# Performance work log

Measured on AMD Instinct MI355X. Metric: run time of the kernel, lower is better.

## Reference

```python
import jax, jax.numpy as jnp
import numpy as np

N = 50000      # nodes
E = 400000     # edges (before self-loops)
IN = 128
HID = 64
HEADS = 8
OUT = 3
NEG_SLOPE = 0.2
EPS = 1e-6


def setup_inputs() -> dict:
    key = jax.random.key(0)
    ks = jax.random.split(key, 32)
    def nrm(k, shape, s=0.05):
        return jax.random.normal(k, shape, dtype=jnp.float32) * s
    inp = {}
    inp['x'] = nrm(ks[0], (N, IN), 1.0)
    inp['edge_index'] = jax.random.randint(ks[1], (2, E), 0, N)
    inp['res_W'] = nrm(ks[2], (OUT, IN))
    inp['res_b'] = jnp.zeros((OUT,), jnp.float32)
    # (in, out, heads, concat) per GAT layer
    dims = [(IN, HID, HEADS, True), (HID * HEADS, HID, HEADS, True),
            (HID * HEADS, HID, HEADS, True), (HID * HEADS, OUT, 1, False)]
    j = 3
    for i, (ci, co, h, cc) in enumerate(dims):
        inp['ln_g%d' % i] = jnp.ones((ci,), jnp.float32)
        inp['ln_b%d' % i] = jnp.zeros((ci,), jnp.float32)
        inp['W%d' % i] = nrm(ks[j], (h * co, ci)); j += 1
        inp['asr%d' % i] = nrm(ks[j], (h, co)); j += 1
        inp['adt%d' % i] = nrm(ks[j], (h, co)); j += 1
        inp['b%d' % i] = jnp.zeros((h * co if cc else co,), jnp.float32)
    return inp


def layer_norm(x, g, b):
    mu = x.mean(-1, keepdims=True)
    var = ((x - mu) ** 2).mean(-1, keepdims=True)
    return (x - mu) / jnp.sqrt(var + EPS) * g + b


def gat_conv(x, src, dst, W, a_src, a_dst, bias, heads, co, concat):
    n = x.shape[0]
    h = (x @ W.T).reshape(n, heads, co)                    # [N,H,C]
    al_src = jnp.sum(h * a_src, axis=-1)                   # [N,H]
    al_dst = jnp.sum(h * a_dst, axis=-1)                   # [N,H]
    e = jax.nn.leaky_relu(al_src[src] + al_dst[dst], NEG_SLOPE)  # [E',H]
    # segment softmax over incoming edges of each destination node
    m = jax.ops.segment_max(e, dst, num_segments=n)
    e = jnp.exp(e - m[dst])
    s = jax.ops.segment_sum(e, dst, num_segments=n)
    alpha = e / s[dst]                                     # [E',H]
    msg = h[src] * alpha[..., None]                        # [E',H,C]
    out = jax.ops.segment_sum(msg, dst, num_segments=n)    # [N,H,C]
    out = out.reshape(n, heads * co) if concat else out.mean(axis=1)
    return out + bias


def reference(x, edge_index, res_W, res_b,
              ln_g0, ln_b0, W0, asr0, adt0, b0,
              ln_g1, ln_b1, W1, asr1, adt1, b1,
              ln_g2, ln_b2, W2, asr2, adt2, b2,
              ln_g3, ln_b3, W3, asr3, adt3, b3):
    n = x.shape[0]
    loops = jnp.arange(n)
    src = jnp.concatenate([edge_index[0], loops])          # add self-loops (PyG default)
    dst = jnp.concatenate([edge_index[1], loops])
    residual = x @ res_W.T + res_b
    layers = [(ln_g0, ln_b0, W0, asr0, adt0, b0, HEADS, HID, True),
              (ln_g1, ln_b1, W1, asr1, adt1, b1, HEADS, HID, True),
              (ln_g2, ln_b2, W2, asr2, adt2, b2, HEADS, HID, True),
              (ln_g3, ln_b3, W3, asr3, adt3, b3, 1, OUT, False)]
    h = x
    num_layers = len(layers)
    for i, (g, bb, W, a_s, a_d, bi, hd, co, cc) in enumerate(layers):
        x_res = h
        h = layer_norm(h, g, bb)
        h = gat_conv(h, src, dst, W, a_s, a_d, bi, hd, co, cc)
        if i < num_layers - 1:
            h = jax.nn.gelu(h, approximate=False)
            if h.shape == x_res.shape:
                h = h + x_res
    return h + residual
```

## Files before the change

kernel.cpp:

```cpp
#include <hip/hip_runtime.h>
#include <math.h>

#define NN 50000
#define MPAD 50048
#define EE 400000
#define NE 450000
#define IN_F 128
#define NEG_SLOPE 0.2f
#define EPSV 1e-6f

typedef unsigned short bf16u;
typedef short bf8_t __attribute__((ext_vector_type(8)));
typedef float f32x4 __attribute__((ext_vector_type(4)));

__device__ __forceinline__ float bf2f(unsigned int u) {
    return __uint_as_float(u << 16);
}
__device__ __forceinline__ float bf2f_hi(unsigned int u) {
    return __uint_as_float(u & 0xFFFF0000u);
}
__device__ __forceinline__ bf16u f2bf(float f) {
    unsigned int u = __float_as_uint(f);
    unsigned int r = (u + 0x7FFFu + ((u >> 16) & 1u)) >> 16;
    return (bf16u)r;
}
__device__ __forceinline__ float gelu_f(float v) {
    return 0.5f * v * (1.0f + erff(v * 0.70710678118654752f));
}

__device__ __forceinline__ void gload_lds16(const void* g, void* l) {
    __builtin_amdgcn_global_load_lds(
        (__attribute__((address_space(1))) void*)(g),
        (__attribute__((address_space(3))) void*)(l), 16, 0, 0);
}

__global__ void k_zero_i32(int* p, int n) {
    int i = blockIdx.x * 256 + threadIdx.x;
    if (i < n) p[i] = 0;
}

__global__ void k_deg(const int* __restrict__ ei, int* __restrict__ deg) {
    int i = blockIdx.x * 256 + threadIdx.x;
    if (i >= NE) return;
    int d = (i < EE) ? ei[EE + i] : (i - EE);
    atomicAdd(&deg[d], 1);
}

__global__ __launch_bounds__(256) void k_scan1(const int* __restrict__ deg,
                                               int* __restrict__ incl,
                                               int* __restrict__ bsums, int n) {
    __shared__ int sm[1024];
    int base = blockIdx.x * 1024;
    for (int i = threadIdx.x; i < 1024; i += 256)
        sm[i] = (base + i < n) ? deg[base + i] : 0;
    __syncthreads();
    for (int off = 1; off < 1024; off <<= 1) {
        int v[4];
#pragma unroll
        for (int j = 0; j < 4; j++) {
            int i = threadIdx.x + 256 * j;
            v[j] = (i >= off) ? sm[i - off] : 0;
        }
        __syncthreads();
#pragma unroll
        for (int j = 0; j < 4; j++) {
            int i = threadIdx.x + 256 * j;
            sm[i] += v[j];
        }
        __syncthreads();
    }
    for (int i = threadIdx.x; i < 1024; i += 256)
        if (base + i < n) incl[base + i] = sm[i];
    if (threadIdx.x == 0) bsums[blockIdx.x] = sm[1023];
}

__global__ void k_scan2(int* bsums, int nb) {
    if (threadIdx.x == 0 && blockIdx.x == 0) {
        int run = 0;
        for (int i = 0; i < nb; i++) { int v = bsums[i]; bsums[i] = run; run += v; }
    }
}

__global__ void k_scan3(const int* __restrict__ deg, int* __restrict__ rowptr,
                        int* __restrict__ cursor, const int* __restrict__ bsums,
                        int n, int ne) {
    int i = blockIdx.x * 256 + threadIdx.x;
    if (i < n) {
        int excl = rowptr[i] + bsums[i >> 10] - deg[i];
        rowptr[i] = excl;
        cursor[i] = excl;
    }
    if (i == n) rowptr[n] = ne;
}

__global__ void k_scatter(const int* __restrict__ ei, int* __restrict__ cursor,
                          int* __restrict__ col) {
    int i = blockIdx.x * 256 + threadIdx.x;
    if (i >= NE) return;
    int s, d;
    if (i < EE) { s = ei[i]; d = ei[EE + i]; }
    else        { s = i - EE; d = i - EE; }
    int p = atomicAdd(&cursor[d], 1);
    col[p] = s;
}

__global__ void k_cast(const float* __restrict__ x, bf16u* __restrict__ h, int total) {
    int i = blockIdx.x * 256 + threadIdx.x;
    if (i < total) h[i] = f2bf(x[i]);
}

__global__ __launch_bounds__(256) void k_castres(const float* __restrict__ x,
                                                 const float* __restrict__ rw,
                                                 const float* __restrict__ rb,
                                                 bf16u* __restrict__ h,
                                                 float* __restrict__ stats,
                                                 float* __restrict__ res, int n) {
    int row = (blockIdx.x * 256 + threadIdx.x) >> 6;
    int lane = threadIdx.x & 63;
    if (row >= n) return;
    float2 v = *(const float2*)(x + (size_t)row * 128 + lane * 2);
    unsigned int pk = (unsigned int)f2bf(v.x) | ((unsigned int)f2bf(v.y) << 16);
    *(unsigned int*)(h + (size_t)row * 128 + lane * 2) = pk;
    float2 w0 = *(const float2*)(rw + 0 * 128 + lane * 2);
    float2 w1 = *(const float2*)(rw + 1 * 128 + lane * 2);
    float2 w2 = *(const float2*)(rw + 2 * 128 + lane * 2);
    float s = v.x + v.y, s2 = v.x * v.x + v.y * v.y;
    float a0 = v.x * w0.x + v.y * w0.y;
    float a1 = v.x * w1.x + v.y * w1.y;
    float a2 = v.x * w2.x + v.y * w2.y;
#pragma unroll
    for (int off = 32; off; off >>= 1) {
        s  += __shfl_xor(s, off);
        s2 += __shfl_xor(s2, off);
        a0 += __shfl_xor(a0, off);
        a1 += __shfl_xor(a1, off);
        a2 += __shfl_xor(a2, off);
    }
    if (lane == 0) {
        float mu = s * (1.0f / 128.0f);
        float var = s2 * (1.0f / 128.0f) - mu * mu;
        stats[row * 2 + 0] = mu;
        stats[row * 2 + 1] = rsqrtf(var + EPSV);
        res[row * 3 + 0] = a0 + rb[0];
        res[row * 3 + 1] = a1 + rb[1];
        res[row * 3 + 2] = a2 + rb[2];
    }
}

#define BM 128
#define BN 128
#define BKK 32
__global__ __launch_bounds__(256) void k_gemm_mfma(const bf16u* __restrict__ H,
                                                   const float* __restrict__ stats,
                                                   const float* __restrict__ g,
                                                   const float* __restrict__ bbias,
                                                   const bf16u* __restrict__ Wb,
                                                   bf16u* __restrict__ C,
                                                   const float* __restrict__ asr,
                                                   const float* __restrict__ adt,
                                                   float* __restrict__ alsrc,
                                                   float* __restrict__ aldst,
                                                   int Mreal, int ci, int K) {
    __shared__ __align__(16) bf16u As[BM * BKK];
    __shared__ __align__(16) bf16u Bs[BN * BKK];
    const int tid = threadIdx.x;
    const int w = tid >> 6, lane = tid & 63;
    const int row0 = blockIdx.x * BM, col0 = blockIdx.y * BN;
    const int wr = (w >> 1) * 64, wc = (w & 1) * 64;

    const int srow = w * 32 + (lane >> 2);
    const int scol = (lane & 3) * 8;
    const bf16u* gA = H + (size_t)(row0 + srow) * ci + scol;
    const bf16u* gB = Wb + (size_t)(col0 + srow) * ci + scol;
    const float mu1 = stats[(row0 + srow) * 2 + 0];
    const float rs1 = stats[(row0 + srow) * 2 + 1];
    const float mu2 = stats[(row0 + srow + 16) * 2 + 0];
    const float rs2 = stats[(row0 + srow + 16) * 2 + 1];
    bf16u* lA1 = &As[(size_t)srow * BKK + scol];
    bf16u* lA2 = &As[(size_t)(srow + 16) * BKK + scol];
    void* lB1 = &Bs[(size_t)(w * 32) * BKK];
    void* lB2 = &Bs[(size_t)(w * 32 + 16) * BKK];

    f32x4 acc[4][4] = {};

    const int fr = lane & 15;
    const int fk = (lane >> 4) * 8;

    for (int k0 = 0; k0 < ci; k0 += BKK) {
        uint4 ra1 = *(const uint4*)(gA + k0);
        uint4 ra2 = *(const uint4*)(gA + (size_t)16 * ci + k0);
        float4 g0 = *(const float4*)(g + k0 + scol);
        float4 g1 = *(const float4*)(g + k0 + scol + 4);
        float4 b0 = *(const float4*)(bbias + k0 + scol);
        float4 b1 = *(const float4*)(bbias + k0 + scol + 4);
        float gg[8] = {g0.x, g0.y, g0.z, g0.w, g1.x, g1.y, g1.z, g1.w};
        float bb[8] = {b0.x, b0.y, b0.z, b0.w, b1.x, b1.y, b1.z, b1.w};
        unsigned int u1[4] = {ra1.x, ra1.y, ra1.z, ra1.w};
        unsigned int u2[4] = {ra2.x, ra2.y, ra2.z, ra2.w};
        uint4 p1, p2;
        {
            unsigned int po[4], qo[4];
#pragma unroll
            for (int j = 0; j < 4; j++) {
                float va = (bf2f(u1[j] & 0xFFFFu) - mu1) * rs1;
                float vb = (bf2f_hi(u1[j])         - mu1) * rs1;
                float oa = fmaf(va, gg[2 * j], bb[2 * j]);
                float ob = fmaf(vb, gg[2 * j + 1], bb[2 * j + 1]);
                po[j] = (unsigned int)f2bf(oa) | ((unsigned int)f2bf(ob) << 16);
                float vc = (bf2f(u2[j] & 0xFFFFu) - mu2) * rs2;
                float vd = (bf2f_hi(u2[j])         - mu2) * rs2;
                float oc = fmaf(vc, gg[2 * j], bb[2 * j]);
                float od = fmaf(vd, gg[2 * j + 1], bb[2 * j + 1]);
                qo[j] = (unsigned int)f2bf(oc) | ((unsigned int)f2bf(od) << 16);
            }
            p1 = make_uint4(po[0], po[1], po[2], po[3]);
            p2 = make_uint4(qo[0], qo[1], qo[2], qo[3]);
        }

        __syncthreads();
        *(uint4*)lA1 = p1;
        *(uint4*)lA2 = p2;
        gload_lds16(gB + k0, lB1);
        gload_lds16(gB + (size_t)16 * ci + k0, lB2);
        __syncthreads();

        bf8_t af[4], bf[4];
#pragma unroll
        for (int m = 0; m < 4; m++)
            af[m] = *(const bf8_t*)&As[(size_t)(wr + m * 16 + fr) * BKK + fk];
#pragma unroll
        for (int n = 0; n < 4; n++)
            bf[n] = *(const bf8_t*)&Bs[(size_t)(wc + n * 16 + fr) * BKK + fk];
#pragma unroll
        for (int m = 0; m < 4; m++)
#pragma unroll
            for (int n = 0; n < 4; n++)
                acc[m][n] = __builtin_amdgcn_mfma_f32_16x16x32_bf16(af[m], bf[n], acc[m][n], 0, 0, 0);
    }

    const int fc = lane & 15;
    const int fq = (lane >> 4) * 4;

#pragma unroll
    for (int m = 0; m < 4; m++) {
#pragma unroll
        for (int r = 0; r < 4; r++) {
            int row = row0 + wr + m * 16 + fq + r;
            if (row >= Mreal) continue;
#pragma unroll
            for (int n = 0; n < 4; n++) {
                int col = col0 + wc + n * 16 + fc;
                C[(size_t)row * K + col] = f2bf(acc[m][n][r]);
            }
        }
    }

    const int head = blockIdx.y * 2 + (wc >> 6);
    float av[4], dv[4];
#pragma unroll
    for (int n = 0; n < 4; n++) {
        av[n] = asr[head * 64 + n * 16 + fc];
        dv[n] = adt[head * 64 + n * 16 + fc];
    }
#pragma unroll
    for (int m = 0; m < 4; m++) {
#pragma unroll
        for (int r = 0; r < 4; r++) {
            float s1 = acc[m][0][r] * av[0] + acc[m][1][r] * av[1]
                     + acc[m][2][r] * av[2] + acc[m][3][r] * av[3];
            float s2 = acc[m][0][r] * dv[0] + acc[m][1][r] * dv[1]
                     + acc[m][2][r] * dv[2] + acc[m][3][r] * dv[3];
#pragma unroll
            for (int o = 1; o < 16; o <<= 1) {
                s1 += __shfl_xor(s1, o);
                s2 += __shfl_xor(s2, o);
            }
            int row = row0 + wr + m * 16 + fq + r;
            if (fc == 0 && row < Mreal) {
                alsrc[row * 8 + head] = s1;
                aldst[row * 8 + head] = s2;
            }
        }
    }
}

__global__ __launch_bounds__(256) void k_lin3(const bf16u* __restrict__ h,
                                              const float* __restrict__ stats,
                                              const float* __restrict__ g,
                                              const float* __restrict__ bb,
                                              const float* __restrict__ W,
                                              const float* __restrict__ a_s,
                                              const float* __restrict__ a_d,
                                              bf16u* __restrict__ hlin3,
                                              float* __restrict__ alsrc,
                                              float* __restrict__ aldst, int n) {
    int row = (blockIdx.x * 256 + threadIdx.x) >> 6;
    int lane = threadIdx.x & 63;
    if (row >= n) return;
    float mu = stats[row * 2 + 0], rs = stats[row * 2 + 1];
    uint4 r = *(const uint4*)(h + (size_t)row * 512 + lane * 8);
    float4 g0 = *(const float4*)(g + lane * 8);
    float4 g1 = *(const float4*)(g + lane * 8 + 4);
    float4 b0 = *(const float4*)(bb + lane * 8);
    float4 b1 = *(const float4*)(bb + lane * 8 + 4);
    float gg[8] = {g0.x, g0.y, g0.z, g0.w, g1.x, g1.y, g1.z, g1.w};
    float bv[8] = {b0.x, b0.y, b0.z, b0.w, b1.x, b1.y, b1.z, b1.w};
    unsigned int u[4] = {r.x, r.y, r.z, r.w};
    float ln[8];
#pragma unroll
    for (int j = 0; j < 4; j++) {
        ln[2 * j]     = fmaf((bf2f(u[j] & 0xFFFFu) - mu) * rs, gg[2 * j], bv[2 * j]);
        ln[2 * j + 1] = fmaf((bf2f_hi(u[j])         - mu) * rs, gg[2 * j + 1], bv[2 * j + 1]);
    }
    float a0 = 0.f, a1 = 0.f, a2 = 0.f;
#pragma unroll
    for (int j = 0; j < 8; j++) {
        int k = lane * 8 + j;
        a0 += ln[j] * W[k];
        a1 += ln[j] * W[512 + k];
        a2 += ln[j] * W[1024 + k];
    }
#pragma unroll
    for (int off = 32; off; off >>= 1) {
        a0 += __shfl_down(a0, off);
        a1 += __shfl_down(a1, off);
        a2 += __shfl_down(a2, off);
    }
    if (lane == 0) {
        *(unsigned int*)(hlin3 + (size_t)row * 4) =
            (unsigned int)f2bf(a0) | ((unsigned int)f2bf(a1) << 16);
        *(unsigned int*)(hlin3 + (size_t)row * 4 + 2) = (unsigned int)f2bf(a2);
        alsrc[row] = a0 * a_s[0] + a1 * a_s[1] + a2 * a_s[2];
        aldst[row] = a0 * a_d[0] + a1 * a_d[1] + a2 * a_d[2];
    }
}

__global__ __launch_bounds__(256) void k_aggN(const bf16u* __restrict__ hlin,
                                              const float* __restrict__ alsrc,
                                              const float* __restrict__ aldst,
                                              const int* __restrict__ rowptr,
                                              const int* __restrict__ col,
                                              const float* __restrict__ bias,
                                              bf16u* __restrict__ hio,
                                              float* __restrict__ stats,
                                              int n, int dores) {
    __shared__ uint2 aldsU[4][8][66];
    int wv = threadIdx.x >> 6;
    int node = (blockIdx.x * 256 + threadIdx.x) >> 6;
    int lane = threadIdx.x & 63;
    if (node >= n) return;
    int beg = rowptr[node], end = rowptr[node + 1];
    int deg = end - beg;

    const float4* dvv = (const float4*)(aldst + node * 8);
    float4 da = dvv[0], db = dvv[1];
    float ad[8] = {da.x, da.y, da.z, da.w, db.x, db.y, db.z, db.w};

    float s = 0.f, s2 = 0.f;

    if (deg <= 64) {
        unsigned int offb = 0;
        float raw[8];
#pragma unroll
        for (int h = 0; h < 8; h++) raw[h] = -INFINITY;
        if (lane < deg) {
            int srcreg = col[beg + lane];
            offb = (unsigned int)srcreg << 10;
            const float4* sv = (const float4*)(alsrc + srcreg * 8);
            float4 sa = sv[0], sb = sv[1];
            float sl[8] = {sa.x, sa.y, sa.z, sa.w, sb.x, sb.y, sb.z, sb.w};
#pragma unroll
            for (int h = 0; h < 8; h++) {
                float v = sl[h] + ad[h];
                raw[h] = (v >= 0.f) ? v : NEG_SLOPE * v;
            }
        }
        float m[8];
#pragma unroll
        for (int h = 0; h < 8; h++) m[h] = raw[h];
#pragma unroll
        for (int off = 32; off; off >>= 1)
#pragma unroll
            for (int h = 0; h < 8; h++) m[h] = fmaxf(m[h], __shfl_xor(m[h], off));
        float ex[8], sm[8];
#pragma unroll
        for (int h = 0; h < 8; h++) {
            ex[h] = (lane < deg) ? __expf(raw[h] - m[h]) : 0.f;
            sm[h] = ex[h];
        }
#pragma unroll
        for (int off = 32; off; off >>= 1)
#pragma unroll
            for (int h = 0; h < 8; h++) sm[h] += __shfl_xor(sm[h], off);
#pragma unroll
        for (int h = 0; h < 8; h++) {
            uint2 t;
            t.x = __float_as_uint(ex[h] * (1.0f / sm[h]));
            t.y = offb;
            aldsU[wv][h][lane] = t;
        }
        asm volatile("s_waitcnt lgkmcnt(0)" ::: "memory");

        int hl = lane >> 3;
        const uint2* myal = &aldsU[wv][hl][0];
        const char* base2 = (const char*)hlin + (lane << 4);
        float acc[8] = {};
        int e = 0;
        for (; e + 2 <= deg; e += 2) {
            uint2 t0 = myal[e];
            uint2 t1 = myal[e + 1];
            uint4 u0 = *(const uint4*)(base2 + t0.y);
            uint4 u1 = *(const uint4*)(base2 + t1.y);
            float a0 = __uint_as_float(t0.x), a1 = __uint_as_float(t1.x);
            acc[0] = fmaf(a0, bf2f(u0.x & 0xFFFFu), acc[0]);
            acc[1] = fmaf(a0, bf2f_hi(u0.x),        acc[1]);
            acc[2] = fmaf(a0, bf2f(u0.y & 0xFFFFu), acc[2]);
            acc[3] = fmaf(a0, bf2f_hi(u0.y),        acc[3]);
            acc[4] = fmaf(a0, bf2f(u0.z & 0xFFFFu), acc[4]);
            acc[5] = fmaf(a0, bf2f_hi(u0.z),        acc[5]);
            acc[6] = fmaf(a0, bf2f(u0.w & 0xFFFFu), acc[6]);
            acc[7] = fmaf(a0, bf2f_hi(u0.w),        acc[7]);
            acc[0] = fmaf(a1, bf2f(u1.x & 0xFFFFu), acc[0]);
            acc[1] = fmaf(a1, bf2f_hi(u1.x),        acc[1]);
            acc[2] = fmaf(a1, bf2f(u1.y & 0xFFFFu), acc[2]);
            acc[3] = fmaf(a1, bf2f_hi(u1.y),        acc[3]);
            acc[4] = fmaf(a1, bf2f(u1.z & 0xFFFFu), acc[4]);
            acc[5] = fmaf(a1, bf2f_hi(u1.z),        acc[5]);
            acc[6] = fmaf(a1, bf2f(u1.w & 0xFFFFu), acc[6]);
            acc[7] = fmaf(a1, bf2f_hi(u1.w),        acc[7]);
        }
        if (e < deg) {
            uint2 t0 = myal[e];
            uint4 u0 = *(const uint4*)(base2 + t0.y);
            float a0 = __uint_as_float(t0.x);
            acc[0] = fmaf(a0, bf2f(u0.x & 0xFFFFu), acc[0]);
            acc[1] = fmaf(a0, bf2f_hi(u0.x),        acc[1]);
            acc[2] = fmaf(a0, bf2f(u0.y & 0xFFFFu), acc[2]);
            acc[3] = fmaf(a0, bf2f_hi(u0.y),        acc[3]);
            acc[4] = fmaf(a0, bf2f(u0.z & 0xFFFFu), acc[4]);
            acc[5] = fmaf(a0, bf2f_hi(u0.z),        acc[5]);
            acc[6] = fmaf(a0, bf2f(u0.w & 0xFFFFu), acc[6]);
            acc[7] = fmaf(a0, bf2f_hi(u0.w),        acc[7]);
        }

        size_t idx = (size_t)node * 512 + lane * 8;
        float4 b0 = *(const float4*)(bias + lane * 8);
        float4 b1 = *(const float4*)(bias + lane * 8 + 4);
        float bb[8] = {b0.x, b0.y, b0.z, b0.w, b1.x, b1.y, b1.z, b1.w};
        float fin[8];
#pragma unroll
        for (int j = 0; j < 8; j++) fin[j] = gelu_f(acc[j] + bb[j]);
        if (dores) {
            uint4 up = *(const uint4*)(hio + idx);
            fin[0] += bf2f(up.x & 0xFFFFu); fin[1] += bf2f_hi(up.x);
            fin[2] += bf2f(up.y & 0xFFFFu); fin[3] += bf2f_hi(up.y);
            fin[4] += bf2f(up.z & 0xFFFFu); fin[5] += bf2f_hi(up.z);
            fin[6] += bf2f(up.w & 0xFFFFu); fin[7] += bf2f_hi(up.w);
        }
        uint4 pk;
        pk.x = (unsigned int)f2bf(fin[0]) | ((unsigned int)f2bf(fin[1]) << 16);
        pk.y = (unsigned int)f2bf(fin[2]) | ((unsigned int)f2bf(fin[3]) << 16);
        pk.z = (unsigned int)f2bf(fin[4]) | ((unsigned int)f2bf(fin[5]) << 16);
        pk.w = (unsigned int)f2bf(fin[6]) | ((unsigned int)f2bf(fin[7]) << 16);
        *(uint4*)(hio + idx) = pk;
#pragma unroll
        for (int j = 0; j < 8; j++) { s += fin[j]; s2 += fin[j] * fin[j]; }
    } else {
        for (int h = 0; h < 8; h++) {
            float adh = ad[h];
            float m = -INFINITY;
            for (int e = beg + lane; e < end; e += 64) {
                float v = alsrc[col[e] * 8 + h] + adh;
                v = (v >= 0.f) ? v : NEG_SLOPE * v;
                m = fmaxf(m, v);
            }
#pragma unroll
            for (int off = 32; off; off >>= 1) m = fmaxf(m, __shfl_xor(m, off));
            float sum = 0.f;
            for (int e = beg + lane; e < end; e += 64) {
                float v = alsrc[col[e] * 8 + h] + adh;
                v = (v >= 0.f) ? v : NEG_SLOPE * v;
                sum += __expf(v - m);
            }
#pragma unroll
            for (int off = 32; off; off >>= 1) sum += __shfl_xor(sum, off);
            float inv = 1.0f / sum;
            float acc = 0.f;
            for (int e = beg; e < end; e++) {
                int src = col[e];
                float v = alsrc[src * 8 + h] + adh;
                v = (v >= 0.f) ? v : NEG_SLOPE * v;
                float alpha = __expf(v - m) * inv;
                acc = fmaf(alpha, bf2f(hlin[((size_t)src << 9) + h * 64 + lane]), acc);
            }
            float fin = gelu_f(acc + bias[h * 64 + lane]);
            size_t idx = (size_t)node * 512 + h * 64 + lane;
            if (dores) fin += bf2f(hio[idx]);
            hio[idx] = f2bf(fin);
            s += fin; s2 += fin * fin;
        }
    }

#pragma unroll
    for (int off = 32; off; off >>= 1) {
        s  += __shfl_xor(s, off);
        s2 += __shfl_xor(s2, off);
    }
    if (lane == 0) {
        float mu = s * (1.0f / 512.0f);
        float var = s2 * (1.0f / 512.0f) - mu * mu;
        stats[node * 2 + 0] = mu;
        stats[node * 2 + 1] = rsqrtf(var + EPSV);
    }
}

__global__ __launch_bounds__(256) void k_aggF(const bf16u* __restrict__ hlin3,
                                              const float* __restrict__ alsrc,
                                              const float* __restrict__ aldst,
                                              const int* __restrict__ rowptr,
                                              const int* __restrict__ col,
                                              const float* __restrict__ bias,
                                              float* __restrict__ outf,
                                              const float* __restrict__ resid, int n) {
    int node = (blockIdx.x * 256 + threadIdx.x) >> 6;
    int lane = threadIdx.x & 63;
    if (node >= n) return;
    int beg = rowptr[node], end = rowptr[node + 1];
    int deg = end - beg;
    float adh = aldst[node];

    if (deg <= 64) {
        int src = 0;
        float raw = -INFINITY;
        if (lane < deg) {
            src = col[beg + lane];
            float v = alsrc[src] + adh;
            raw = (v >= 0.f) ? v : NEG_SLOPE * v;
        }
        float m = raw;
#pragma unroll
        for (int off = 32; off; off >>= 1) m = fmaxf(m, __shfl_xor(m, off));
        float ex = (lane < deg) ? __expf(raw - m) : 0.f;
        float sum = ex;
#pragma unroll
        for (int off = 32; off; off >>= 1) sum += __shfl_xor(sum, off);
        float alpha = ex / sum;

        float c0 = 0.f, c1 = 0.f, c2 = 0.f;
        if (lane < deg) {
            uint2 u = *(const uint2*)(hlin3 + (size_t)src * 4);
            c0 = alpha * bf2f(u.x & 0xFFFFu);
            c1 = alpha * bf2f_hi(u.x);
            c2 = alpha * bf2f(u.y & 0xFFFFu);
        }
#pragma unroll
        for (int off = 32; off; off >>= 1) {
            c0 += __shfl_xor(c0, off);
            c1 += __shfl_xor(c1, off);
            c2 += __shfl_xor(c2, off);
        }
        if (lane == 0) {
            outf[node * 3 + 0] = c0 + bias[0] + resid[node * 3 + 0];
            outf[node * 3 + 1] = c1 + bias[1] + resid[node * 3 + 1];
            outf[node * 3 + 2] = c2 + bias[2] + resid[node * 3 + 2];
        }
    } else {
        float m = -INFINITY;
        for (int e = beg + lane; e < end; e += 64) {
            float v = alsrc[col[e]] + adh;
            v = (v >= 0.f) ? v : NEG_SLOPE * v;
            m = fmaxf(m, v);
        }
#pragma unroll
        for (int off = 32; off; off >>= 1) m = fmaxf(m, __shfl_xor(m, off));
        float sum = 0.f;
        for (int e = beg + lane; e < end; e += 64) {
            float v = alsrc[col[e]] + adh;
            v = (v >= 0.f) ? v : NEG_SLOPE * v;
            sum += __expf(v - m);
        }
#pragma unroll
        for (int off = 32; off; off >>= 1) sum += __shfl_xor(sum, off);
        float inv = 1.0f / sum;
        float acc = 0.f;
        for (int e = beg; e < end; e++) {
            int src = col[e];
            float v = alsrc[src] + adh;
            v = (v >= 0.f) ? v : NEG_SLOPE * v;
            float alpha = __expf(v - m) * inv;
            if (lane < 3) acc += alpha * bf2f(hlin3[(size_t)src * 4 + lane]);
        }
        if (lane < 3)
            outf[node * 3 + lane] = acc + bias[lane] + resid[node * 3 + lane];
    }
}

extern "C" void kernel_launch(void* const* d_in, const int* in_sizes, int n_in,
                              void* d_out, int out_size, void* d_ws, size_t ws_size,
                              hipStream_t stream) {
    const float* x    = (const float*)d_in[0];
    const int*   ei   = (const int*)d_in[1];
    const float* resW = (const float*)d_in[2];
    const float* resb = (const float*)d_in[3];
    const float *lng[4], *lnb[4], *Wm[4], *asr[4], *adt[4], *bias[4];
    int idx = 4;
    for (int i = 0; i < 4; i++) {
        lng[i]  = (const float*)d_in[idx++];
        lnb[i]  = (const float*)d_in[idx++];
        Wm[i]   = (const float*)d_in[idx++];
        asr[i]  = (const float*)d_in[idx++];
        adt[i]  = (const float*)d_in[idx++];
        bias[i] = (const float*)d_in[idx++];
    }

    char* base = (char*)d_ws;
    size_t off = 0;
    auto alloc = [&](size_t bytes) {
        void* p = base + off;
        off += (bytes + 255) & ~(size_t)255;
        return p;
    };
    bf16u* hbuf  = (bf16u*)alloc((size_t)MPAD * 512 * 2);
    bf16u* lbuf  = (bf16u*)alloc((size_t)MPAD * 512 * 2);
    bf16u* wb0   = (bf16u*)alloc((size_t)512 * 128 * 2);
    bf16u* wb1   = (bf16u*)alloc((size_t)512 * 512 * 2);
    bf16u* wb2   = (bf16u*)alloc((size_t)512 * 512 * 2);
    float* stats = (float*)alloc((size_t)MPAD * 2 * 4);
    float* alsrc = (float*)alloc((size_t)NN * 8 * 4);
    float* aldst = (float*)alloc((size_t)NN * 8 * 4);
    float* resid = (float*)alloc((size_t)NN * 3 * 4);
    int* rowptr  = (int*)alloc((size_t)(NN + 1) * 4);
    int* cursor  = (int*)alloc((size_t)NN * 4);
    int* deg     = (int*)alloc((size_t)NN * 4);
    int* colidx  = (int*)alloc((size_t)NE * 4);
    int* bsums   = (int*)alloc(256 * 4);
    if (off > ws_size) return;

    float* out = (float*)d_out;

    k_zero_i32<<<(NN + 255) / 256, 256, 0, stream>>>(deg, NN);
    k_deg<<<(NE + 255) / 256, 256, 0, stream>>>(ei, deg);
    int nb = (NN + 1023) / 1024;
    k_scan1<<<nb, 256, 0, stream>>>(deg, rowptr, bsums, NN);
    k_scan2<<<1, 64, 0, stream>>>(bsums, nb);
    k_scan3<<<(NN + 1 + 255) / 256, 256, 0, stream>>>(deg, rowptr, cursor, bsums, NN, NE);
    k_scatter<<<(NE + 255) / 256, 256, 0, stream>>>(ei, cursor, colidx);

    int rowBlocks = (NN * 64 + 255) / 256;
    k_castres<<<rowBlocks, 256, 0, stream>>>(x, resW, resb, hbuf, stats, resid, NN);
    k_cast<<<(512 * 128 + 255) / 256, 256, 0, stream>>>(Wm[0], wb0, 512 * 128);
    k_cast<<<(512 * 512 + 255) / 256, 256, 0, stream>>>(Wm[1], wb1, 512 * 512);
    k_cast<<<(512 * 512 + 255) / 256, 256, 0, stream>>>(Wm[2], wb2, 512 * 512);

    const bf16u* wb[3] = {wb0, wb1, wb2};
    const int ci_a[3] = {128, 512, 512};

    for (int i = 0; i < 3; i++) {
        int ci = ci_a[i];
        int dores = (i >= 1) ? 1 : 0;

        dim3 ggrid(MPAD / BM, 512 / BN);
        k_gemm_mfma<<<ggrid, 256, 0, stream>>>(hbuf, stats, lng[i], lnb[i], wb[i],
                                               lbuf, asr[i], adt[i], alsrc, aldst,
                                               NN, ci, 512);

        k_aggN<<<rowBlocks, 256, 0, stream>>>(lbuf, alsrc, aldst, rowptr, colidx,
                                              bias[i], hbuf, stats, NN, dores);
    }

    k_lin3<<<rowBlocks, 256, 0, stream>>>(hbuf, stats, lng[3], lnb[3], Wm[3],
                                          asr[3], adt[3], lbuf, alsrc, aldst, NN);
    k_aggF<<<rowBlocks, 256, 0, stream>>>(lbuf, alsrc, aldst, rowptr, colidx,
                                          bias[3], out, resid, NN);
}
```

Baseline: 670.1 us.

## Move LayerNorm into aggregation epilogue and double-buffer the MFMA GEMM

The aggregation kernels now apply the next layer's LayerNorm themselves and write a normalized bf16 activation buffer. This lets the GEMM load A tiles straight to LDS with global_load_lds instead of normalizing them in registers. The GEMM uses a BK=64 double-buffered LDS pipeline with XOR swizzle to hide load latency and avoid bank conflicts. The cost is an extra 512-wide bf16 write per node per layer plus a larger workspace. LeakyReLU is also simplified to a max-based form.

```diff
diff --git a/kernel.cpp b/kernel.cpp
--- a/kernel.cpp
+++ b/kernel.cpp
@@ -26,6 +26,9 @@
 }
 __device__ __forceinline__ float gelu_f(float v) {
     return 0.5f * v * (1.0f + erff(v * 0.70710678118654752f));
+}
+__device__ __forceinline__ float lrelu(float v) {
+    return fmaxf(v, NEG_SLOPE * v);
 }
 
 __device__ __forceinline__ void gload_lds16(const void* g, void* l) {
@@ -109,18 +112,17 @@
     if (i < total) h[i] = f2bf(x[i]);
 }
 
-__global__ __launch_bounds__(256) void k_castres(const float* __restrict__ x,
-                                                 const float* __restrict__ rw,
-                                                 const float* __restrict__ rb,
-                                                 bf16u* __restrict__ h,
-                                                 float* __restrict__ stats,
-                                                 float* __restrict__ res, int n) {
+__global__ __launch_bounds__(256) void k_castres2(const float* __restrict__ x,
+                                                  const float* __restrict__ rw,
+                                                  const float* __restrict__ rb,
+                                                  const float* __restrict__ g0,
+                                                  const float* __restrict__ b0,
+                                                  bf16u* __restrict__ abuf,
+                                                  float* __restrict__ res, int n) {
     int row = (blockIdx.x * 256 + threadIdx.x) >> 6;
     int lane = threadIdx.x & 63;
     if (row >= n) return;
     float2 v = *(const float2*)(x + (size_t)row * 128 + lane * 2);
-    unsigned int pk = (unsigned int)f2bf(v.x) | ((unsigned int)f2bf(v.y) << 16);
-    *(unsigned int*)(h + (size_t)row * 128 + lane * 2) = pk;
     float2 w0 = *(const float2*)(rw + 0 * 128 + lane * 2);
     float2 w1 = *(const float2*)(rw + 1 * 128 + lane * 2);
     float2 w2 = *(const float2*)(rw + 2 * 128 + lane * 2);
@@ -136,11 +138,16 @@
         a1 += __shfl_xor(a1, off);
         a2 += __shfl_xor(a2, off);
     }
+    float mu = s * (1.0f / 128.0f);
+    float var = s2 * (1.0f / 128.0f) - mu * mu;
+    float rs = rsqrtf(var + EPSV);
+    float2 gg = *(const float2*)(g0 + lane * 2);
+    float2 bb = *(const float2*)(b0 + lane * 2);
+    float l0 = fmaf((v.x - mu) * rs, gg.x, bb.x);
+    float l1 = fmaf((v.y - mu) * rs, gg.y, bb.y);
+    *(unsigned int*)(abuf + (size_t)row * 128 + lane * 2) =
+        (unsigned int)f2bf(l0) | ((unsigned int)f2bf(l1) << 16);
     if (lane == 0) {
-        float mu = s * (1.0f / 128.0f);
-        float var = s2 * (1.0f / 128.0f) - mu * mu;
-        stats[row * 2 + 0] = mu;
-        stats[row * 2 + 1] = rsqrtf(var + EPSV);
         res[row * 3 + 0] = a0 + rb[0];
         res[row * 3 + 1] = a1 + rb[1];
         res[row * 3 + 2] = a2 + rb[2];
@@ -149,93 +156,67 @@
 
 #define BM 128
 #define BN 128
-#define BKK 32
-__global__ __launch_bounds__(256) void k_gemm_mfma(const bf16u* __restrict__ H,
-                                                   const float* __restrict__ stats,
-                                                   const float* __restrict__ g,
-                                                   const float* __restrict__ bbias,
-                                                   const bf16u* __restrict__ Wb,
-                                                   bf16u* __restrict__ C,
-                                                   const float* __restrict__ asr,
-                                                   const float* __restrict__ adt,
-                                                   float* __restrict__ alsrc,
-                                                   float* __restrict__ aldst,
-                                                   int Mreal, int ci, int K) {
-    __shared__ __align__(16) bf16u As[BM * BKK];
-    __shared__ __align__(16) bf16u Bs[BN * BKK];
+#define BK2 64
+__global__ __launch_bounds__(256) void k_gemm_db(const bf16u* __restrict__ A,
+                                                 const bf16u* __restrict__ Wb,
+                                                 bf16u* __restrict__ C,
+                                                 const float* __restrict__ asr,
+                                                 const float* __restrict__ adt,
+                                                 float* __restrict__ alsrc,
+                                                 float* __restrict__ aldst,
+                                                 int Mreal, int ci, int K) {
+    __shared__ __align__(16) bf16u As[2][BM * BK2];
+    __shared__ __align__(16) bf16u Bs[2][BN * BK2];
     const int tid = threadIdx.x;
     const int w = tid >> 6, lane = tid & 63;
     const int row0 = blockIdx.x * BM, col0 = blockIdx.y * BN;
     const int wr = (w >> 1) * 64, wc = (w & 1) * 64;
 
-    const int srow = w * 32 + (lane >> 2);
-    const int scol = (lane & 3) * 8;
-    const bf16u* gA = H + (size_t)(row0 + srow) * ci + scol;
-    const bf16u* gB = Wb + (size_t)(col0 + srow) * ci + scol;
-    const float mu1 = stats[(row0 + srow) * 2 + 0];
-    const float rs1 = stats[(row0 + srow) * 2 + 1];
-    const float mu2 = stats[(row0 + srow + 16) * 2 + 0];
-    const float rs2 = stats[(row0 + srow + 16) * 2 + 1];
-    bf16u* lA1 = &As[(size_t)srow * BKK + scol];
-    bf16u* lA2 = &As[(size_t)(srow + 16) * BKK + scol];
-    void* lB1 = &Bs[(size_t)(w * 32) * BKK];
-    void* lB2 = &Bs[(size_t)(w * 32 + 16) * BKK];
+    const int lrow = lane >> 3;
+    const int scolx = ((lane & 7) * 8) ^ (lrow << 3);
+    const bf16u* gA = A + (size_t)(row0 + w * 32 + lrow) * ci + scolx;
+    const bf16u* gB = Wb + (size_t)(col0 + w * 32 + lrow) * ci + scolx;
+
+    const int nk = ci / BK2;
+
+#pragma unroll
+    for (int j = 0; j < 4; j++) {
+        gload_lds16(gA + (size_t)(j * 8) * ci, &As[0][(w * 32 + j * 8) * BK2]);
+        gload_lds16(gB + (size_t)(j * 8) * ci, &Bs[0][(w * 32 + j * 8) * BK2]);
+    }
+    __syncthreads();
 
     f32x4 acc[4][4] = {};
-
     const int fr = lane & 15;
     const int fk = (lane >> 4) * 8;
-
-    for (int k0 = 0; k0 < ci; k0 += BKK) {
-        uint4 ra1 = *(const uint4*)(gA + k0);
-        uint4 ra2 = *(const uint4*)(gA + (size_t)16 * ci + k0);
-        float4 g0 = *(const float4*)(g + k0 + scol);
-        float4 g1 = *(const float4*)(g + k0 + scol + 4);
-        float4 b0 = *(const float4*)(bbias + k0 + scol);
-        float4 b1 = *(const float4*)(bbias + k0 + scol + 4);
-        float gg[8] = {g0.x, g0.y, g0.z, g0.w, g1.x, g1.y, g1.z, g1.w};
-        float bb[8] = {b0.x, b0.y, b0.z, b0.w, b1.x, b1.y, b1.z, b1.w};
-        unsigned int u1[4] = {ra1.x, ra1.y, ra1.z, ra1.w};
-        unsigned int u2[4] = {ra2.x, ra2.y, ra2.z, ra2.w};
-        uint4 p1, p2;
-        {
-            unsigned int po[4], qo[4];
+    const int fxor = (fr & 7) << 3;
+
+    for (int t = 0; t < nk; t++) {
+        const int cur = t & 1;
+        if (t + 1 < nk) {
+            const int k0 = (t + 1) * BK2;
 #pragma unroll
             for (int j = 0; j < 4; j++) {
-                float va = (bf2f(u1[j] & 0xFFFFu) - mu1) * rs1;
-                float vb = (bf2f_hi(u1[j])         - mu1) * rs1;
-                float oa = fmaf(va, gg[2 * j], bb[2 * j]);
-                float ob = fmaf(vb, gg[2 * j + 1], bb[2 * j + 1]);
-                po[j] = (unsigned int)f2bf(oa) | ((unsigned int)f2bf(ob) << 16);
-                float vc = (bf2f(u2[j] & 0xFFFFu) - mu2) * rs2;
-                float vd = (bf2f_hi(u2[j])         - mu2) * rs2;
-                float oc = fmaf(vc, gg[2 * j], bb[2 * j]);
-                float od = fmaf(vd, gg[2 * j + 1], bb[2 * j + 1]);
-                qo[j] = (unsigned int)f2bf(oc) | ((unsigned int)f2bf(od) << 16);
+                gload_lds16(gA + (size_t)(j * 8) * ci + k0, &As[cur ^ 1][(w * 32 + j * 8) * BK2]);
+                gload_lds16(gB + (size_t)(j * 8) * ci + k0, &Bs[cur ^ 1][(w * 32 + j * 8) * BK2]);
             }
-            p1 = make_uint4(po[0], po[1], po[2], po[3]);
-            p2 = make_uint4(qo[0], qo[1], qo[2], qo[3]);
-        }
-
-        __syncthreads();
-        *(uint4*)lA1 = p1;
-        *(uint4*)lA2 = p2;
-        gload_lds16(gB + k0, lB1);
-        gload_lds16(gB + (size_t)16 * ci + k0, lB2);
-        __syncthreads();
-
-        bf8_t af[4], bf[4];
-#pragma unroll
-        for (int m = 0; m < 4; m++)
-            af[m] = *(const bf8_t*)&As[(size_t)(wr + m * 16 + fr) * BKK + fk];
-#pragma unroll
-        for (int n = 0; n < 4; n++)
-            bf[n] = *(const bf8_t*)&Bs[(size_t)(wc + n * 16 + fr) * BKK + fk];
-#pragma unroll
-        for (int m = 0; m < 4; m++)
+        }
+#pragma unroll
+        for (int ks = 0; ks < 2; ks++) {
+            bf8_t af[4], bfv[4];
+#pragma unroll
+            for (int m = 0; m < 4; m++)
+                af[m] = *(const bf8_t*)&As[cur][(wr + m * 16 + fr) * BK2 + ((ks * 32 + fk) ^ fxor)];
 #pragma unroll
             for (int n = 0; n < 4; n++)
-                acc[m][n] = __builtin_amdgcn_mfma_f32_16x16x32_bf16(af[m], bf[n], acc[m][n], 0, 0, 0);
+                bfv[n] = *(const bf8_t*)&Bs[cur][(wc + n * 16 + fr) * BK2 + ((ks * 32 + fk) ^ fxor)];
+#pragma unroll
+            for (int m = 0; m < 4; m++)
+#pragma unroll
+                for (int n = 0; n < 4; n++)
+                    acc[m][n] = __builtin_amdgcn_mfma_f32_16x16x32_bf16(af[m], bfv[n], acc[m][n], 0, 0, 0);
+        }
+        if (t + 1 < nk) __syncthreads();
     }
 
     const int fc = lane & 15;
@@ -284,33 +265,23 @@
     }
 }
 
-__global__ __launch_bounds__(256) void k_lin3(const bf16u* __restrict__ h,
-                                              const float* __restrict__ stats,
-                                              const float* __restrict__ g,
-                                              const float* __restrict__ bb,
-                                              const float* __restrict__ W,
-                                              const float* __restrict__ a_s,
-                                              const float* __restrict__ a_d,
-                                              bf16u* __restrict__ hlin3,
-                                              float* __restrict__ alsrc,
-                                              float* __restrict__ aldst, int n) {
+__global__ __launch_bounds__(256) void k_lin3b(const bf16u* __restrict__ an,
+                                               const float* __restrict__ W,
+                                               const float* __restrict__ a_s,
+                                               const float* __restrict__ a_d,
+                                               bf16u* __restrict__ hlin3,
+                                               float* __restrict__ alsrc,
+                                               float* __restrict__ aldst, int n) {
     int row = (blockIdx.x * 256 + threadIdx.x) >> 6;
     int lane = threadIdx.x & 63;
     if (row >= n) return;
-    float mu = stats[row * 2 + 0], rs = stats[row * 2 + 1];
-    uint4 r = *(const uint4*)(h + (size_t)row * 512 + lane * 8);
-    float4 g0 = *(const float4*)(g + lane * 8);
-    float4 g1 = *(const float4*)(g + lane * 8 + 4);
-    float4 b0 = *(const float4*)(bb + lane * 8);
-    float4 b1 = *(const float4*)(bb + lane * 8 + 4);
-    float gg[8] = {g0.x, g0.y, g0.z, g0.w, g1.x, g1.y, g1.z, g1.w};
-    float bv[8] = {b0.x, b0.y, b0.z, b0.w, b1.x, b1.y, b1.z, b1.w};
+    uint4 r = *(const uint4*)(an + (size_t)row * 512 + lane * 8);
     unsigned int u[4] = {r.x, r.y, r.z, r.w};
     float ln[8];
 #pragma unroll
     for (int j = 0; j < 4; j++) {
-        ln[2 * j]     = fmaf((bf2f(u[j] & 0xFFFFu) - mu) * rs, gg[2 * j], bv[2 * j]);
-        ln[2 * j + 1] = fmaf((bf2f_hi(u[j])         - mu) * rs, gg[2 * j + 1], bv[2 * j + 1]);
+        ln[2 * j]     = bf2f(u[j] & 0xFFFFu);
+        ln[2 * j + 1] = bf2f_hi(u[j]);
     }
     float a0 = 0.f, a1 = 0.f, a2 = 0.f;
 #pragma unroll
@@ -335,15 +306,17 @@
     }
 }
 
-__global__ __launch_bounds__(256) void k_aggN(const bf16u* __restrict__ hlin,
-                                              const float* __restrict__ alsrc,
-                                              const float* __restrict__ aldst,
-                                              const int* __restrict__ rowptr,
-                                              const int* __restrict__ col,
-                                              const float* __restrict__ bias,
-                                              bf16u* __restrict__ hio,
-                                              float* __restrict__ stats,
-                                              int n, int dores) {
+__global__ __launch_bounds__(256) void k_aggN2(const bf16u* __restrict__ hlin,
+                                               const float* __restrict__ alsrc,
+                                               const float* __restrict__ aldst,
+                                               const int* __restrict__ rowptr,
+                                               const int* __restrict__ col,
+                                               const float* __restrict__ bias,
+                                               bf16u* __restrict__ hio,
+                                               const float* __restrict__ gn,
+                                               const float* __restrict__ bn,
+                                               bf16u* __restrict__ abuf,
+                                               int n, int dores) {
     __shared__ uint2 aldsU[4][8][66];
     int wv = threadIdx.x >> 6;
     int node = (blockIdx.x * 256 + threadIdx.x) >> 6;
@@ -357,6 +330,7 @@
     float ad[8] = {da.x, da.y, da.z, da.w, db.x, db.y, db.z, db.w};
 
     float s = 0.f, s2 = 0.f;
+    float fin[8];
 
     if (deg <= 64) {
         unsigned int offb = 0;
@@ -370,10 +344,7 @@
             float4 sa = sv[0], sb = sv[1];
             float sl[8] = {sa.x, sa.y, sa.z, sa.w, sb.x, sb.y, sb.z, sb.w};
 #pragma unroll
-            for (int h = 0; h < 8; h++) {
-                float v = sl[h] + ad[h];
-                raw[h] = (v >= 0.f) ? v : NEG_SLOPE * v;
-            }
+            for (int h = 0; h < 8; h++) raw[h] = lrelu(sl[h] + ad[h]);
         }
         float m[8];
 #pragma unroll
@@ -447,7 +418,6 @@
         float4 b0 = *(const float4*)(bias + lane * 8);
         float4 b1 = *(const float4*)(bias + lane * 8 + 4);
         float bb[8] = {b0.x, b0.y, b0.z, b0.w, b1.x, b1.y, b1.z, b1.w};
-        float fin[8];
 #pragma unroll
         for (int j = 0; j < 8; j++) fin[j] = gelu_f(acc[j] + bb[j]);
         if (dores) {
@@ -465,52 +435,68 @@
         *(uint4*)(hio + idx) = pk;
 #pragma unroll
         for (int j = 0; j < 8; j++) { s += fin[j]; s2 += fin[j] * fin[j]; }
+
+#pragma unroll
+        for (int off = 32; off; off >>= 1) {
+            s  += __shfl_xor(s, off);
+            s2 += __shfl_xor(s2, off);
+        }
+        float mu = s * (1.0f / 512.0f);
+        float rs = rsqrtf(s2 * (1.0f / 512.0f) - mu * mu + EPSV);
+        float4 g0 = *(const float4*)(gn + lane * 8);
+        float4 g1 = *(const float4*)(gn + lane * 8 + 4);
+        float4 n0 = *(const float4*)(bn + lane * 8);
+        float4 n1 = *(const float4*)(bn + lane * 8 + 4);
+        float gg[8] = {g0.x, g0.y, g0.z, g0.w, g1.x, g1.y, g1.z, g1.w};
+        float nb[8] = {n0.x, n0.y, n0.z, n0.w, n1.x, n1.y, n1.z, n1.w};
+        float lnv[8];
+#pragma unroll
+        for (int j = 0; j < 8; j++) lnv[j] = fmaf((fin[j] - mu) * rs, gg[j], nb[j]);
+        uint4 pl;
+        pl.x = (unsigned int)f2bf(lnv[0]) | ((unsigned int)f2bf(lnv[1]) << 16);
+        pl.y = (unsigned int)f2bf(lnv[2]) | ((unsigned int)f2bf(lnv[3]) << 16);
+        pl.z = (unsigned int)f2bf(lnv[4]) | ((unsigned int)f2bf(lnv[5]) << 16);
+        pl.w = (unsigned int)f2bf(lnv[6]) | ((unsigned int)f2bf(lnv[7]) << 16);
+        *(uint4*)(abuf + idx) = pl;
     } else {
+        float fins[8];
         for (int h = 0; h < 8; h++) {
             float adh = ad[h];
             float m = -INFINITY;
-            for (int e = beg + lane; e < end; e += 64) {
-                float v = alsrc[col[e] * 8 + h] + adh;
-                v = (v >= 0.f) ? v : NEG_SLOPE * v;
-                m = fmaxf(m, v);
-            }
+            for (int e = beg + lane; e < end; e += 64)
+                m = fmaxf(m, lrelu(alsrc[col[e] * 8 + h] + adh));
 #pragma unroll
             for (int off = 32; off; off >>= 1) m = fmaxf(m, __shfl_xor(m, off));
             float sum = 0.f;
-            for (int e = beg + lane; e < end; e += 64) {
-                float v = alsrc[col[e] * 8 + h] + adh;
-                v = (v >= 0.f) ? v : NEG_SLOPE * v;
-                sum += __expf(v - m);
-            }
+            for (int e = beg + lane; e < end; e += 64)
+                sum += __expf(lrelu(alsrc[col[e] * 8 + h] + adh) - m);
 #pragma unroll
             for (int off = 32; off; off >>= 1) sum += __shfl_xor(sum, off);
             float inv = 1.0f / sum;
             float acc = 0.f;
             for (int e = beg; e < end; e++) {
                 int src = col[e];
-                float v = alsrc[src * 8 + h] + adh;
-                v = (v >= 0.f) ? v : NEG_SLOPE * v;
-                float alpha = __expf(v - m) * inv;
+                float alpha = __expf(lrelu(alsrc[src * 8 + h] + adh) - m) * inv;
                 acc = fmaf(alpha, bf2f(hlin[((size_t)src << 9) + h * 64 + lane]), acc);
             }
-            float fin = gelu_f(acc + bias[h * 64 + lane]);
+            float fv = gelu_f(acc + bias[h * 64 + lane]);
             size_t idx = (size_t)node * 512 + h * 64 + lane;
-            if (dores) fin += bf2f(hio[idx]);
-            hio[idx] = f2bf(fin);
-            s += fin; s2 += fin * fin;
-        }
-    }
-
-#pragma unroll
-    for (int off = 32; off; off >>= 1) {
-        s  += __shfl_xor(s, off);
-        s2 += __shfl_xor(s2, off);
-    }
-    if (lane == 0) {
+            if (dores) fv += bf2f(hio[idx]);
+            hio[idx] = f2bf(fv);
+            fins[h] = fv;
+            s += fv; s2 += fv * fv;
+        }
+#pragma unroll
+        for (int off = 32; off; off >>= 1) {
+            s  += __shfl_xor(s, off);
+            s2 += __shfl_xor(s2, off);
+        }
         float mu = s * (1.0f / 512.0f);
-        float var = s2 * (1.0f / 512.0f) - mu * mu;
-        stats[node * 2 + 0] = mu;
-        stats[node * 2 + 1] = rsqrtf(var + EPSV);
+        float rs = rsqrtf(s2 * (1.0f / 512.0f) - mu * mu + EPSV);
+        for (int h = 0; h < 8; h++) {
+            int c = h * 64 + lane;
+            abuf[(size_t)node * 512 + c] = f2bf(fmaf((fins[h] - mu) * rs, gn[c], bn[c]));
+        }
     }
 }
 
@@ -534,8 +520,7 @@
         float raw = -INFINITY;
         if (lane < deg) {
             src = col[beg + lane];
-            float v = alsrc[src] + adh;
-            raw = (v >= 0.f) ? v : NEG_SLOPE * v;
+            raw = lrelu(alsrc[src] + adh);
         }
         float m = raw;
 #pragma unroll
@@ -566,28 +551,20 @@
         }
     } else {
         float m = -INFINITY;
-        for (int e = beg + lane; e < end; e += 64) {
-            float v = alsrc[col[e]] + adh;
-            v = (v >= 0.f) ? v : NEG_SLOPE * v;
-            m = fmaxf(m, v);
-        }
+        for (int e = beg + lane; e < end; e += 64)
+            m = fmaxf(m, lrelu(alsrc[col[e]] + adh));
 #pragma unroll
         for (int off = 32; off; off >>= 1) m = fmaxf(m, __shfl_xor(m, off));
         float sum = 0.f;
-        for (int e = beg + lane; e < end; e += 64) {
-            float v = alsrc[col[e]] + adh;
-            v = (v >= 0.f) ? v : NEG_SLOPE * v;
-            sum += __expf(v - m);
-        }
+        for (int e = beg + lane; e < end; e += 64)
+            sum += __expf(lrelu(alsrc[col[e]] + adh) - m);
 #pragma unroll
         for (int off = 32; off; off >>= 1) sum += __shfl_xor(sum, off);
         float inv = 1.0f / sum;
         float acc = 0.f;
         for (int e = beg; e < end; e++) {
             int src = col[e];
-            float v = alsrc[src] + adh;
-            v = (v >= 0.f) ? v : NEG_SLOPE * v;
-            float alpha = __expf(v - m) * inv;
+            float alpha = __expf(lrelu(alsrc[src] + adh) - m) * inv;
             if (lane < 3) acc += alpha * bf2f(hlin3[(size_t)src * 4 + lane]);
         }
         if (lane < 3)
@@ -620,12 +597,6 @@
         off += (bytes + 255) & ~(size_t)255;
         return p;
     };
-    bf16u* hbuf  = (bf16u*)alloc((size_t)MPAD * 512 * 2);
-    bf16u* lbuf  = (bf16u*)alloc((size_t)MPAD * 512 * 2);
-    bf16u* wb0   = (bf16u*)alloc((size_t)512 * 128 * 2);
-    bf16u* wb1   = (bf16u*)alloc((size_t)512 * 512 * 2);
-    bf16u* wb2   = (bf16u*)alloc((size_t)512 * 512 * 2);
-    float* stats = (float*)alloc((size_t)MPAD * 2 * 4);
     float* alsrc = (float*)alloc((size_t)NN * 8 * 4);
     float* aldst = (float*)alloc((size_t)NN * 8 * 4);
     float* resid = (float*)alloc((size_t)NN * 3 * 4);
@@ -634,6 +605,12 @@
     int* deg     = (int*)alloc((size_t)NN * 4);
     int* colidx  = (int*)alloc((size_t)NE * 4);
     int* bsums   = (int*)alloc(256 * 4);
+    bf16u* wb0   = (bf16u*)alloc((size_t)512 * 128 * 2);
+    bf16u* wb1   = (bf16u*)alloc((size_t)512 * 512 * 2);
+    bf16u* wb2   = (bf16u*)alloc((size_t)512 * 512 * 2);
+    bf16u* hbuf  = (bf16u*)alloc((size_t)MPAD * 512 * 2);
+    bf16u* lbuf  = (bf16u*)alloc((size_t)MPAD * 512 * 2);
+    bf16u* abuf  = (bf16u*)alloc((size_t)MPAD * 512 * 2);
     if (off > ws_size) return;
 
     float* out = (float*)d_out;
@@ -647,29 +624,27 @@
     k_scatter<<<(NE + 255) / 256, 256, 0, stream>>>(ei, cursor, colidx);
 
     int rowBlocks = (NN * 64 + 255) / 256;
-    k_castres<<<rowBlocks, 256, 0, stream>>>(x, resW, resb, hbuf, stats, resid, NN);
     k_cast<<<(512 * 128 + 255) / 256, 256, 0, stream>>>(Wm[0], wb0, 512 * 128);
     k_cast<<<(512 * 512 + 255) / 256, 256, 0, stream>>>(Wm[1], wb1, 512 * 512);
     k_cast<<<(512 * 512 + 255) / 256, 256, 0, stream>>>(Wm[2], wb2, 512 * 512);
 
     const bf16u* wb[3] = {wb0, wb1, wb2};
     const int ci_a[3] = {128, 512, 512};
-
+    dim3 ggrid(MPAD / BM, 512 / BN);
+
+    k_castres2<<<rowBlocks, 256, 0, stream>>>(x, resW, resb, lng[0], lnb[0],
+                                              abuf, resid, NN);
     for (int i = 0; i < 3; i++) {
-        int ci = ci_a[i];
         int dores = (i >= 1) ? 1 : 0;
-
-        dim3 ggrid(MPAD / BM, 512 / BN);
-        k_gemm_mfma<<<ggrid, 256, 0, stream>>>(hbuf, stats, lng[i], lnb[i], wb[i],
-                                               lbuf, asr[i], adt[i], alsrc, aldst,
-                                               NN, ci, 512);
-
-        k_aggN<<<rowBlocks, 256, 0, stream>>>(lbuf, alsrc, aldst, rowptr, colidx,
-                                              bias[i], hbuf, stats, NN, dores);
-    }
-
-    k_lin3<<<rowBlocks, 256, 0, stream>>>(hbuf, stats, lng[3], lnb[3], Wm[3],
-                                          asr[3], adt[3], lbuf, alsrc, aldst, NN);
+        k_gemm_db<<<ggrid, 256, 0, stream>>>(abuf, wb[i], lbuf,
+                                             asr[i], adt[i], alsrc, aldst,
+                                             NN, ci_a[i], 512);
+        k_aggN2<<<rowBlocks, 256, 0, stream>>>(lbuf, alsrc, aldst, rowptr, colidx,
+                                               bias[i], hbuf, lng[i + 1], lnb[i + 1],
+                                               abuf, NN, dores);
+    }
+    k_lin3b<<<rowBlocks, 256, 0, stream>>>(abuf, Wm[3], asr[3], adt[3],
+                                           lbuf, alsrc, aldst, NN);
     k_aggF<<<rowBlocks, 256, 0, stream>>>(lbuf, alsrc, aldst, rowptr, colidx,
                                           bias[3], out, resid, NN);
 }
```

Measured after the change: 664.9 us. Within noise of the previous version (-0.8%).
